# Kernel tuning notes

Measured on AMD Instinct MI355X. Metric: run time of the kernel, lower is better.

## Reference

```python
import jax, jax.numpy as jnp
import numpy as np

B, L, D = 2, 2048, 2048
H = 16
DH = D // H  # 128
EPS = 1e-6


def _rope_cos_sin(seq_len, dim, dtype):
    inv_freq = 1.0 / (10000.0 ** (jnp.arange(0, dim, 2, dtype=jnp.float32) / dim))
    t = jnp.arange(seq_len, dtype=jnp.float32)
    freqs = jnp.einsum('i,j->ij', t, inv_freq)          # [L, dim/2]
    emb = jnp.concatenate([freqs, freqs], axis=-1)      # [L, dim]
    return jnp.cos(emb).astype(dtype)[None, None], jnp.sin(emb).astype(dtype)[None, None]


def _rotate_half(x):
    x1, x2 = jnp.split(x, 2, axis=-1)
    return jnp.concatenate([-x2, x1], axis=-1)


def _rms_norm(x, w):
    var = jnp.mean(jnp.square(x), axis=-1, keepdims=True)
    return x * jax.lax.rsqrt(var + EPS) * w


def setup_inputs() -> dict:
    key = jax.random.key(0)
    ks = jax.random.split(key, 4)
    s_in = 1.0 / np.sqrt(D)
    return {
        'x': jax.random.normal(ks[0], (B, L, D), jnp.float32),
        'attention_mask': jnp.zeros((B, 1, 1, L), jnp.bool_),
        'Wqkv': jax.random.normal(ks[1], (D, 3 * D), jnp.float32) * s_in,
        'bqkv': jnp.zeros((3 * D,), jnp.float32),
        'Wout': jax.random.normal(ks[2], (D, D), jnp.float32) * s_in,
        'bout': jnp.zeros((D,), jnp.float32),
        'q_norm_w': jnp.ones((DH,), jnp.float32),
        'k_norm_w': jnp.ones((DH,), jnp.float32),
    }


def reference(x, attention_mask, Wqkv, bqkv, Wout, bout, q_norm_w, k_norm_w):
    b, l, d = x.shape
    qkv = x @ Wqkv + bqkv                                   # [B,L,3D]
    q, k, v = jnp.split(qkv, 3, axis=-1)
    # [B,H,L,DH]
    q = q.reshape(b, l, H, DH).transpose(0, 2, 1, 3)
    k = k.reshape(b, l, H, DH).transpose(0, 2, 1, 3)
    v = v.reshape(b, l, H, DH).transpose(0, 2, 1, 3)

    cos, sin = _rope_cos_sin(l, DH, x.dtype)
    q = q * cos + _rotate_half(q) * sin
    k = k * cos + _rotate_half(k) * sin

    q = _rms_norm(q, q_norm_w)
    k = _rms_norm(k, k_norm_w)

    # SDPA with additive (float-cast) mask, as in the original code
    scale = 1.0 / np.sqrt(DH)
    scores = jnp.einsum('bhqd,bhkd->bhqk', q, k) * scale
    scores = scores + attention_mask.astype(x.dtype)        # broadcast [B,1,1,L]
    attn = jax.nn.softmax(scores, axis=-1)
    out = jnp.einsum('bhqk,bhkd->bhqd', attn, v)            # [B,H,L,DH]

    # zero out masked query rows: padding_mask = mask.transpose(2,3) -> [B,1,L,1]
    padding_mask = jnp.swapaxes(attention_mask, 2, 3)
    out = jnp.where(padding_mask, 0.0, out)

    out = out.transpose(0, 2, 1, 3).reshape(b, l, d)
    return out @ Wout + bout
```

## Files before the change

kernel.cpp:

```cpp
#include <hip/hip_runtime.h>
#include <hip/hip_bf16.h>

typedef __bf16 bf16;
using bf16x8 = __attribute__((ext_vector_type(8))) __bf16;
using bf16x4 = __attribute__((ext_vector_type(4))) __bf16;
using f32x4  = __attribute__((ext_vector_type(4))) float;
using f32x16 = __attribute__((ext_vector_type(16))) float;

#define DEV __device__ __forceinline__

DEV void load_lds16(const void* g, void* l) {
  __builtin_amdgcn_global_load_lds(
      (const __attribute__((address_space(1))) void*)g,
      (__attribute__((address_space(3))) void*)l, 16, 0, 0);
}

__global__ __launch_bounds__(256) void k_prep(
    const float* __restrict__ x, bf16* __restrict__ xb,
    const float* __restrict__ Wq, bf16* __restrict__ wqT,
    const float* __restrict__ Wo, bf16* __restrict__ woT,
    float* __restrict__ invf) {
  __shared__ float t[64][65];
  int bid = blockIdx.x;
  int tid = threadIdx.x;
  if (bid < 4096) {
    long i = ((long)bid * 256 + tid) * 8;
    float4 a = *(const float4*)(x + i);
    float4 b = *(const float4*)(x + i + 4);
    bf16x8 o;
    o[0] = (bf16)a.x; o[1] = (bf16)a.y; o[2] = (bf16)a.z; o[3] = (bf16)a.w;
    o[4] = (bf16)b.x; o[5] = (bf16)b.y; o[6] = (bf16)b.z; o[7] = (bf16)b.w;
    *(bf16x8*)(xb + i) = o;
    return;
  }
  if (bid >= 8192) {
    if (tid < 64) invf[tid] = 1.0f / (float)pow(10000.0, (double)tid / 64.0);
    return;
  }
  const float* in;
  bf16* out;
  int R, C, rb;
  if (bid < 7168) { in = Wq; out = wqT; R = 2048; C = 6144; rb = bid - 4096; }
  else            { in = Wo; out = woT; R = 2048; C = 2048; rb = bid - 7168; }
  int nbc = C >> 6;
  long r0 = (long)(rb / nbc) * 64, c0 = (long)(rb % nbc) * 64;
#pragma unroll
  for (int i = 0; i < 4; ++i) {
    int ch = tid + i * 256;
    int r = ch >> 4, c4 = (ch & 15) * 4;
    float4 v = *(const float4*)(in + (r0 + r) * C + c0 + c4);
    t[r][c4] = v.x; t[r][c4 + 1] = v.y; t[r][c4 + 2] = v.z; t[r][c4 + 3] = v.w;
  }
  __syncthreads();
#pragma unroll
  for (int i = 0; i < 2; ++i) {
    int ch = tid + i * 256;
    int c = ch >> 3, r8 = (ch & 7) * 8;
    bf16x8 o;
#pragma unroll
    for (int j = 0; j < 8; ++j) o[j] = (bf16)t[r8 + j][c];
    *(bf16x8*)(out + (c0 + c) * R + r0 + r8) = o;
  }
}

template <typename OutT>
__global__ __launch_bounds__(256) void k_gemm_bt(
    const bf16* __restrict__ A, const bf16* __restrict__ Bt,
    const float* __restrict__ bias, OutT* __restrict__ C,
    int M, int N, int K, int fuse,
    const float* __restrict__ invf,
    const float* __restrict__ qw, const float* __restrict__ kw,
    bf16* __restrict__ q_r, bf16* __restrict__ k_r, bf16* __restrict__ v_t) {
  __shared__ __align__(16) bf16 lAB[2][128 * 64];
  bf16* lA = lAB[0];
  bf16* lB = lAB[1];
  int bid = blockIdx.x;
  if ((gridDim.x & 7) == 0) {
    int q = gridDim.x >> 3;
    bid = (bid & 7) * q + (bid >> 3);
  }
  int nbn = N >> 7;
  int bm = bid / nbn, bn = bid % nbn;
  const int tid = threadIdx.x, lane = tid & 63, wid = tid >> 6;
  const int wr = wid >> 1, wc = wid & 1;
  const int fr = lane & 15, fq = lane >> 4;
  const long abase = (long)bm * 128 * K, bbase = (long)bn * 128 * K;
  f32x4 acc[4][4] = {};

  for (int k0 = 0; k0 < K; k0 += 64) {
    __syncthreads();
#pragma unroll
    for (int it = 0; it < 4; ++it) {
      int ch = it * 256 + tid;
      int r = ch >> 3, u = ch & 7;
      load_lds16(A + abase + (long)r * K + k0 + ((u ^ (r & 7)) << 3), &lA[ch * 8]);
    }
#pragma unroll
    for (int it = 0; it < 4; ++it) {
      int ch = it * 256 + tid;
      int r = ch >> 3, u = ch & 7;
      load_lds16(Bt + bbase + (long)r * K + k0 + ((u ^ (r & 7)) << 3), &lB[ch * 8]);
    }
    __syncthreads();
    bf16x8 af[4][2], bf_[4][2];
#pragma unroll
    for (int m = 0; m < 4; ++m) {
      int R = wr * 64 + m * 16 + fr;
#pragma unroll
      for (int kk = 0; kk < 2; ++kk)
        af[m][kk] = *(const bf16x8*)&lA[R * 64 + (((kk * 4 + fq) ^ (R & 7)) << 3)];
    }
#pragma unroll
    for (int n = 0; n < 4; ++n) {
      int R = wc * 64 + n * 16 + fr;
#pragma unroll
      for (int kk = 0; kk < 2; ++kk)
        bf_[n][kk] = *(const bf16x8*)&lB[R * 64 + (((kk * 4 + fq) ^ (R & 7)) << 3)];
    }
#pragma unroll
    for (int m = 0; m < 4; ++m)
#pragma unroll
      for (int n = 0; n < 4; ++n)
#pragma unroll
        for (int kk = 0; kk < 2; ++kk)
          acc[m][n] = __builtin_amdgcn_mfma_f32_16x16x32_bf16(af[m][kk], bf_[n][kk],
                                                              acc[m][n], 0, 0, 0);
  }

  if (!fuse) {
#pragma unroll
    for (int n = 0; n < 4; ++n) {
      int col = bn * 128 + wc * 64 + n * 16 + fr;
      float bv = bias[col];
#pragma unroll
      for (int m = 0; m < 4; ++m) {
        int row0 = bm * 128 + wr * 64 + m * 16 + fq * 4;
#pragma unroll
        for (int r = 0; r < 4; ++r) {
          float v = acc[m][n][r] + bv;
          C[(long)(row0 + r) * N + col] = (OutT)v;
        }
      }
    }
    return;
  }

  __syncthreads();
  bf16* tile = lAB[0];
  const int h = bn & 15;
  const int b = bm >> 4, l0 = (bm & 15) << 7;

  if (bn < 32) {
#pragma unroll
    for (int n = 0; n < 4; ++n) {
      int col = wc * 64 + n * 16 + fr;
      float bv = bias[bn * 128 + col];
#pragma unroll
      for (int m = 0; m < 4; ++m)
#pragma unroll
        for (int r = 0; r < 4; ++r) {
          int row = wr * 64 + m * 16 + fq * 4 + r;
          tile[row * 128 + (col ^ ((row & 7) << 3))] = (bf16)(acc[m][n][r] + bv);
        }
    }
    __syncthreads();
    const float* wv = (bn < 16) ? qw : kw;
    bf16* dst0 = (bn < 16) ? q_r : k_r;
    const int tcol = tid & 15, rgrp = tid >> 4, i8 = tcol * 8;
    const bool lo = i8 < 64;
    float wvv[8], invv[8];
#pragma unroll
    for (int j = 0; j < 8; ++j) wvv[j] = wv[i8 + j];
#pragma unroll
    for (int j = 0; j < 8; ++j) invv[j] = invf[(i8 + j) & 63];
#pragma unroll
    for (int it = 0; it < 8; ++it) {
      int row = it * 16 + rgrp;
      float fl = (float)(l0 + row);
      float cc[8], sn[8];
#pragma unroll
      for (int j = 0; j < 8; ++j) __sincosf(fl * invv[j], &sn[j], &cc[j]);
      bf16x8 xv = *(const bf16x8*)&tile[row * 128 + (i8 ^ ((row & 7) << 3))];
      float v[8], p[8], rr[8];
      float ss = 0.f;
#pragma unroll
      for (int j = 0; j < 8; ++j) v[j] = (float)xv[j];
#pragma unroll
      for (int j = 0; j < 8; ++j) p[j] = __shfl_xor(v[j], 8);
#pragma unroll
      for (int j = 0; j < 8; ++j) {
        rr[j] = lo ? v[j] * cc[j] - p[j] * sn[j] : v[j] * cc[j] + p[j] * sn[j];
        ss += rr[j] * rr[j];
      }
      ss += __shfl_xor(ss, 1);
      ss += __shfl_xor(ss, 2);
      ss += __shfl_xor(ss, 4);
      ss += __shfl_xor(ss, 8);
      float inv = rsqrtf(ss * (1.f / 128.f) + 1e-6f);
      bf16x8 ov;
#pragma unroll
      for (int j = 0; j < 8; ++j) ov[j] = (bf16)(rr[j] * inv * wvv[j]);
      *(bf16x8*)(dst0 + ((long)((b * 16 + h) * 2048 + (l0 + row))) * 128 + i8) = ov;
    }
  } else {
#pragma unroll
    for (int n = 0; n < 4; ++n) {
      int col = wc * 64 + n * 16 + fr;
      float bv = bias[bn * 128 + col];
#pragma unroll
      for (int m = 0; m < 4; ++m)
#pragma unroll
        for (int r = 0; r < 4; ++r) {
          int row = wr * 64 + m * 16 + fq * 4 + r;
          tile[col * 128 + (row ^ ((col & 7) << 3))] = (bf16)(acc[m][n][r] + bv);
        }
    }
    __syncthreads();
    bf16* dstb = v_t + ((long)((b * 16 + h) * 128)) * 2048 + l0;
#pragma unroll
    for (int it = 0; it < 8; ++it) {
      int ch = it * 256 + tid;
      int d = ch >> 4, l8 = (ch & 15) * 8;
      bf16x8 vv = *(const bf16x8*)&tile[d * 128 + (l8 ^ ((d & 7) << 3))];
      *(bf16x8*)(dstb + (long)d * 2048 + l8) = vv;
    }
  }
}

__global__ __launch_bounds__(512, 1) void k_attn(
    const bf16* __restrict__ q_r, const bf16* __restrict__ k_r,
    const bf16* __restrict__ v_t, const unsigned char* __restrict__ amask,
    bf16* __restrict__ attno) {
  __shared__ __align__(16) bf16 lK[2][64 * 128];
  __shared__ __align__(16) bf16 lV[3][128 * 64];
  __shared__ int sAny;
  const int tid = threadIdx.x, lane = tid & 63, w = tid >> 6;
  const int hi = lane >> 5, q31 = lane & 31;
  const int bh = blockIdx.x & 31, qt = blockIdx.x >> 5;
  const int b = bh >> 4, h = bh & 15;
  const long hbase = (long)bh * 2048 * 128;
  const int q0 = qt * 256 + w * 32;
  const unsigned char* mb = amask + b * 2048;

  if (tid == 0) sAny = 0;
  __syncthreads();
  {
    unsigned mv = *(const unsigned*)(mb + tid * 4);
    if (mv) sAny = 1;
  }

  bf16x8 qf[8];
#pragma unroll
  for (int ksl = 0; ksl < 8; ++ksl)
    qf[ksl] = *(const bf16x8*)(q_r + hbase + (long)(q0 + q31) * 128 + ksl * 16 + hi * 8);

  f32x16 o[4] = {};
  float m_run = -1e30f, l_run = 0.f;
  const float SC2 = 0.08838834764831845f * 1.4426950408889634f;
  const float L2E = 1.4426950408889634f;

#define STAGE_K(buf, kv0)                                                            \
  {                                                                                  \
    _Pragma("unroll") for (int it = 0; it < 2; ++it) {                               \
      int g = it * 512 + w * 64 + lane;                                              \
      int r = g >> 4, u = g & 15;                                                    \
      load_lds16(k_r + hbase + (long)((kv0) + r) * 128 + ((u ^ (r & 7)) << 3),       \
                 &lK[buf][(it * 512 + w * 64) * 8]);                                 \
    }                                                                                \
  }
#define STAGE_V(buf, kv0)                                                            \
  {                                                                                  \
    _Pragma("unroll") for (int it = 0; it < 2; ++it) {                               \
      int g = it * 512 + w * 64 + lane;                                              \
      int r = g >> 3, u = g & 7;                                                     \
      load_lds16(v_t + hbase + (long)r * 2048 + (kv0) + ((u ^ (r & 7)) << 3),        \
                 &lV[buf][(it * 512 + w * 64) * 8]);                                 \
    }                                                                                \
  }

  STAGE_K(0, 0) STAGE_V(0, 0) STAGE_K(1, 64) STAGE_V(1, 64)
  __syncthreads();
  const bool maskAny = sAny != 0;

  f32x16 st0 = {}, st1 = {};
#pragma unroll
  for (int ksl = 0; ksl < 8; ++ksl) {
    const int u = ksl * 2 + hi;
    bf16x8 kf0 = *(const bf16x8*)&lK[0][q31 * 128 + ((u ^ (q31 & 7)) << 3)];
    bf16x8 kf1 = *(const bf16x8*)&lK[0][(32 + q31) * 128 + ((u ^ (q31 & 7)) << 3)];
    st0 = __builtin_amdgcn_mfma_f32_32x32x16_bf16(kf0, qf[ksl], st0, 0, 0, 0);
    st1 = __builtin_amdgcn_mfma_f32_32x32x16_bf16(kf1, qf[ksl], st1, 0, 0, 0);
  }
  __syncthreads();

  for (int t = 0; t < 32; ++t) {
    const int kv0 = t << 6;
    if (t + 2 < 32) {
      STAGE_K(t & 1, kv0 + 128)
      STAGE_V((t + 2) % 3, kv0 + 128)
    }

    f32x16 sn0 = {}, sn1 = {};
    if (t < 31) {
      const bf16* kb = lK[(t + 1) & 1];
#pragma unroll
      for (int ksl = 0; ksl < 8; ++ksl) {
        const int u = ksl * 2 + hi;
        bf16x8 kf0 = *(const bf16x8*)&kb[q31 * 128 + ((u ^ (q31 & 7)) << 3)];
        bf16x8 kf1 = *(const bf16x8*)&kb[(32 + q31) * 128 + ((u ^ (q31 & 7)) << 3)];
        sn0 = __builtin_amdgcn_mfma_f32_32x32x16_bf16(kf0, qf[ksl], sn0, 0, 0, 0);
        sn1 = __builtin_amdgcn_mfma_f32_32x32x16_bf16(kf1, qf[ksl], sn1, 0, 0, 0);
      }
    }

#pragma unroll
    for (int i = 0; i < 16; ++i) { st0[i] *= SC2; st1[i] *= SC2; }
    if (maskAny) {
#pragma unroll
      for (int i = 0; i < 16; ++i) {
        int c = (i & 3) + 8 * (i >> 2) + 4 * hi;
        if (mb[kv0 + c]) st0[i] += L2E;
        if (mb[kv0 + 32 + c]) st1[i] += L2E;
      }
    }
    float tm = st0[0];
#pragma unroll
    for (int i = 1; i < 16; ++i) tm = fmaxf(tm, st0[i]);
#pragma unroll
    for (int i = 0; i < 16; ++i) tm = fmaxf(tm, st1[i]);
    tm = fmaxf(tm, __shfl_xor(tm, 32));

    if (!__all(tm <= m_run + 8.f)) {
      float mn = fmaxf(m_run, tm);
      float corr = exp2f(m_run - mn);
      m_run = mn;
      l_run *= corr;
#pragma unroll
      for (int i = 0; i < 16; ++i) {
        float cr = __shfl(corr, (i & 3) + 8 * (i >> 2) + 4 * hi);
#pragma unroll
        for (int dt = 0; dt < 4; ++dt) o[dt][i] *= cr;
      }
    }

    float rs = 0.f;
#pragma unroll
    for (int i = 0; i < 16; ++i) { st0[i] = exp2f(st0[i] - m_run); rs += st0[i]; }
#pragma unroll
    for (int i = 0; i < 16; ++i) { st1[i] = exp2f(st1[i] - m_run); rs += st1[i]; }
    rs += __shfl_xor(rs, 32);
    l_run += rs;

    union UU { bf16x4 v; uint2 u; };
    union U8 { bf16x8 v; uint4 u; };
    bf16x8 pa[4];
#define MKPA(pidx, STX, bb)                                                          \
  {                                                                                  \
    UU plo, phi;                                                                     \
    plo.v = (bf16x4){(bf16)STX[bb], (bf16)STX[(bb) + 1], (bf16)STX[(bb) + 2],        \
                     (bf16)STX[(bb) + 3]};                                           \
    phi.v = (bf16x4){(bf16)STX[(bb) + 4], (bf16)STX[(bb) + 5], (bf16)STX[(bb) + 6],  \
                     (bf16)STX[(bb) + 7]};                                           \
    unsigned sx = hi ? plo.u.x : phi.u.x, sy = hi ? plo.u.y : phi.u.y;               \
    unsigned rx = (unsigned)__shfl_xor((int)sx, 32), ry = (unsigned)__shfl_xor((int)sy, 32); \
    U8 f;                                                                            \
    f.u.x = hi ? rx : plo.u.x; f.u.y = hi ? ry : plo.u.y;                            \
    f.u.z = hi ? phi.u.x : rx; f.u.w = hi ? phi.u.y : ry;                            \
    pa[pidx] = f.v;                                                                  \
  }
    MKPA(0, st0, 0) MKPA(1, st0, 8) MKPA(2, st1, 0) MKPA(3, st1, 8)
#undef MKPA

    const bf16* vb3 = lV[t % 3];
#pragma unroll
    for (int dt = 0; dt < 4; ++dt) {
      const int dr = dt * 32 + q31;
#pragma unroll
      for (int ks = 0; ks < 4; ++ks) {
        const int u = ks * 2 + hi;
        bf16x8 vb = *(const bf16x8*)&vb3[dr * 64 + ((u ^ (dr & 7)) << 3)];
        o[dt] = __builtin_amdgcn_mfma_f32_32x32x16_bf16(pa[ks], vb, o[dt], 0, 0, 0);
      }
    }

    __syncthreads();
    st0 = sn0;
    st1 = sn1;
  }
#undef STAGE_K
#undef STAGE_V

  float invl = 1.f / l_run;
#pragma unroll
  for (int i = 0; i < 16; ++i) {
    int q = (i & 3) + 8 * (i >> 2) + 4 * hi;
    int qrow = q0 + q;
    float inv = __shfl(invl, q);
    float zm = inv;
    if (maskAny) { if (mb[qrow]) zm = 0.f; }
#pragma unroll
    for (int dt = 0; dt < 4; ++dt)
      attno[(long)(b * 2048 + qrow) * 2048 + h * 128 + dt * 32 + q31] = (bf16)(o[dt][i] * zm);
  }
}

extern "C" void kernel_launch(void* const* d_in, const int* in_sizes, int n_in,
                              void* d_out, int out_size, void* d_ws, size_t ws_size,
                              hipStream_t stream) {
  const float* x = (const float*)d_in[0];
  const unsigned char* amask = (const unsigned char*)d_in[1];
  const float* Wqkv = (const float*)d_in[2];
  const float* bqkv = (const float*)d_in[3];
  const float* Wout = (const float*)d_in[4];
  const float* bout = (const float*)d_in[5];
  const float* qw = (const float*)d_in[6];
  const float* kw = (const float*)d_in[7];
  float* out = (float*)d_out;
  char* ws = (char*)d_ws;

  bf16* xb   = (bf16*)(ws);
  bf16* wqT  = (bf16*)(ws + 16777216);
  bf16* woT  = (bf16*)(ws + 41943040);
  bf16* q_r  = (bf16*)(ws + 100663296);
  bf16* k_r  = (bf16*)(ws + 117440512);
  bf16* v_t  = (bf16*)(ws + 134217728);
  float* invf = (float*)(ws + 150994944);
  bf16* attno = xb;

  k_prep<<<8193, 256, 0, stream>>>(x, xb, Wqkv, wqT, Wout, woT, invf);
  k_gemm_bt<bf16><<<32 * 48, 256, 0, stream>>>(xb, wqT, bqkv, (bf16*)nullptr,
                                               4096, 6144, 2048, 1,
                                               invf, qw, kw, q_r, k_r, v_t);
  k_attn<<<256, 512, 0, stream>>>(q_r, k_r, v_t, amask, attno);
  k_gemm_bt<float><<<32 * 16, 256, 0, stream>>>(attno, woT, bout, out,
                                                4096, 2048, 2048, 0,
                                                nullptr, nullptr, nullptr,
                                                nullptr, nullptr, nullptr);
}
```

Before: 304.2 us.

## Replace QKV GEMM with 256x256-tile, 8-wave, software-pipelined kernel

The fused QKV projection GEMM moves from 128x128 tiles with 4 waves and a load-sync-compute loop to 256x256 tiles with 8 waves. Global-to-LDS loads are double-buffered and interleaved across four compute phases, with explicit vmcnt waits, barriers and setprio around the MFMA bursts. The larger tile cuts global/LDS traffic per flop and hides load latency behind compute. The cost is 128KB of LDS, one block per CU and a grid of only 384 blocks, which may leave the 256 CUs unevenly loaded. The RoPE/RMSNorm and V-transpose epilogues are adapted to cover two heads per tile, and the output GEMM is split into its own non-templated kernel.

```diff
diff --git a/kernel.cpp b/kernel.cpp
--- a/kernel.cpp
+++ b/kernel.cpp
@@ -63,110 +63,107 @@
   }
 }
 
-template <typename OutT>
-__global__ __launch_bounds__(256) void k_gemm_bt(
+__global__ __launch_bounds__(512, 1) void k_gemm8q(
     const bf16* __restrict__ A, const bf16* __restrict__ Bt,
-    const float* __restrict__ bias, OutT* __restrict__ C,
-    int M, int N, int K, int fuse,
+    const float* __restrict__ bias,
     const float* __restrict__ invf,
     const float* __restrict__ qw, const float* __restrict__ kw,
     bf16* __restrict__ q_r, bf16* __restrict__ k_r, bf16* __restrict__ v_t) {
-  __shared__ __align__(16) bf16 lAB[2][128 * 64];
-  bf16* lA = lAB[0];
-  bf16* lB = lAB[1];
+  __shared__ __align__(16) bf16 ls[2][2][256 * 64];
   int bid = blockIdx.x;
-  if ((gridDim.x & 7) == 0) {
-    int q = gridDim.x >> 3;
-    bid = (bid & 7) * q + (bid >> 3);
-  }
-  int nbn = N >> 7;
-  int bm = bid / nbn, bn = bid % nbn;
-  const int tid = threadIdx.x, lane = tid & 63, wid = tid >> 6;
-  const int wr = wid >> 1, wc = wid & 1;
+  { int q = gridDim.x >> 3; bid = (bid & 7) * q + (bid >> 3); }
+  const int bm = bid & 15, bn = bid >> 4;
+  const int tid = threadIdx.x, lane = tid & 63, w = tid >> 6;
+  const int wm = w >> 2, wn = w & 3;
   const int fr = lane & 15, fq = lane >> 4;
-  const long abase = (long)bm * 128 * K, bbase = (long)bn * 128 * K;
-  f32x4 acc[4][4] = {};
-
-  for (int k0 = 0; k0 < K; k0 += 64) {
+  const long abase = (long)bm * 256 * 2048;
+  const long bbase = (long)bn * 256 * 2048;
+  f32x4 acc[8][4] = {};
+  bf16x8 bfv[4][2];
+
+#define STG(op, GP, gb, kt, hf)                                                \
+  { _Pragma("unroll") for (int it2 = 0; it2 < 2; ++it2) {                      \
+      int g = it2 * 512 + tid;                                                 \
+      int rl = g >> 3, u = g & 7;                                              \
+      load_lds16(GP + gb + (long)((hf) * 128 + rl) * 2048 + ((kt) << 6)        \
+                     + ((u ^ (rl & 7)) << 3),                                  \
+                 &ls[op][(kt) & 1][(hf) * 8192 + g * 8]);                      \
+  } }
+
+#define PH(qd, slot, STGCODE)                                                  \
+  {                                                                            \
+    bf16x8 afv[2][2];                                                          \
+    _Pragma("unroll") for (int mm = 0; mm < 2; ++mm)                           \
+      _Pragma("unroll") for (int kk = 0; kk < 2; ++kk) {                       \
+        int R = wm * 128 + ((qd) * 2 + mm) * 16 + fr;                          \
+        afv[mm][kk] = *(const bf16x8*)&ls[0][slot]                             \
+            [R * 64 + (((kk * 4 + fq) ^ (R & 7)) << 3)];                       \
+      }                                                                        \
+    if ((qd) == 0) {                                                           \
+      _Pragma("unroll") for (int nn = 0; nn < 4; ++nn)                         \
+        _Pragma("unroll") for (int kk = 0; kk < 2; ++kk) {                     \
+          int R = wn * 64 + nn * 16 + fr;                                      \
+          bfv[nn][kk] = *(const bf16x8*)&ls[1][slot]                           \
+              [R * 64 + (((kk * 4 + fq) ^ (R & 7)) << 3)];                     \
+        }                                                                      \
+    }                                                                          \
+    STGCODE                                                                    \
+    __builtin_amdgcn_s_barrier();                                              \
+    asm volatile("s_waitcnt lgkmcnt(0)" ::: "memory");                         \
+    __builtin_amdgcn_s_setprio(1);                                             \
+    _Pragma("unroll") for (int mm = 0; mm < 2; ++mm)                           \
+      _Pragma("unroll") for (int nn = 0; nn < 4; ++nn)                         \
+        _Pragma("unroll") for (int kk = 0; kk < 2; ++kk)                       \
+          acc[(qd) * 2 + mm][nn] = __builtin_amdgcn_mfma_f32_16x16x32_bf16(    \
+              afv[mm][kk], bfv[nn][kk], acc[(qd) * 2 + mm][nn], 0, 0, 0);      \
+    __builtin_amdgcn_s_setprio(0);                                             \
+    __builtin_amdgcn_s_barrier();                                              \
+  }
+
+  STG(1, Bt, bbase, 0, 0) STG(1, Bt, bbase, 0, 1)
+  STG(0, A, abase, 0, 0)  STG(0, A, abase, 0, 1)
+  STG(1, Bt, bbase, 1, 0) STG(1, Bt, bbase, 1, 1)
+
+  for (int u = 0; u < 16; ++u) {
+    const int t = 2 * u;
+    asm volatile("s_waitcnt vmcnt(4)" ::: "memory");
+    __builtin_amdgcn_s_barrier();
+    PH(0, 0, STG(0, A, abase, t + 1, 0))
+    PH(1, 0, STG(0, A, abase, t + 1, 1))
+    PH(2, 0, if (u < 15) { STG(1, Bt, bbase, t + 2, 0) })
+    PH(3, 0, if (u < 15) { STG(1, Bt, bbase, t + 2, 1) })
+    if (u < 15) { asm volatile("s_waitcnt vmcnt(4)" ::: "memory"); }
+    else        { asm volatile("s_waitcnt vmcnt(0)" ::: "memory"); }
+    __builtin_amdgcn_s_barrier();
+    PH(0, 1, if (u < 15) { STG(0, A, abase, t + 2, 0) })
+    PH(1, 1, if (u < 15) { STG(0, A, abase, t + 2, 1) })
+    PH(2, 1, if (u < 15) { STG(1, Bt, bbase, t + 3, 0) })
+    PH(3, 1, if (u < 15) { STG(1, Bt, bbase, t + 3, 1) })
+  }
+#undef PH
+#undef STG
+
+  bf16* tile = &ls[0][0][0];
+  const int b = bm >> 3, l0 = (bm & 7) << 8;
+
+  if (bn < 16) {
+#pragma unroll
+    for (int n = 0; n < 4; ++n) {
+      int col = wn * 64 + n * 16 + fr;
+      float bv = bias[bn * 256 + col];
+#pragma unroll
+      for (int m = 0; m < 8; ++m)
+#pragma unroll
+        for (int r = 0; r < 4; ++r) {
+          int row = wm * 128 + m * 16 + fq * 4 + r;
+          tile[row * 256 + (col ^ ((row & 7) << 3))] = (bf16)(acc[m][n][r] + bv);
+        }
+    }
     __syncthreads();
-#pragma unroll
-    for (int it = 0; it < 4; ++it) {
-      int ch = it * 256 + tid;
-      int r = ch >> 3, u = ch & 7;
-      load_lds16(A + abase + (long)r * K + k0 + ((u ^ (r & 7)) << 3), &lA[ch * 8]);
-    }
-#pragma unroll
-    for (int it = 0; it < 4; ++it) {
-      int ch = it * 256 + tid;
-      int r = ch >> 3, u = ch & 7;
-      load_lds16(Bt + bbase + (long)r * K + k0 + ((u ^ (r & 7)) << 3), &lB[ch * 8]);
-    }
-    __syncthreads();
-    bf16x8 af[4][2], bf_[4][2];
-#pragma unroll
-    for (int m = 0; m < 4; ++m) {
-      int R = wr * 64 + m * 16 + fr;
-#pragma unroll
-      for (int kk = 0; kk < 2; ++kk)
-        af[m][kk] = *(const bf16x8*)&lA[R * 64 + (((kk * 4 + fq) ^ (R & 7)) << 3)];
-    }
-#pragma unroll
-    for (int n = 0; n < 4; ++n) {
-      int R = wc * 64 + n * 16 + fr;
-#pragma unroll
-      for (int kk = 0; kk < 2; ++kk)
-        bf_[n][kk] = *(const bf16x8*)&lB[R * 64 + (((kk * 4 + fq) ^ (R & 7)) << 3)];
-    }
-#pragma unroll
-    for (int m = 0; m < 4; ++m)
-#pragma unroll
-      for (int n = 0; n < 4; ++n)
-#pragma unroll
-        for (int kk = 0; kk < 2; ++kk)
-          acc[m][n] = __builtin_amdgcn_mfma_f32_16x16x32_bf16(af[m][kk], bf_[n][kk],
-                                                              acc[m][n], 0, 0, 0);
-  }
-
-  if (!fuse) {
-#pragma unroll
-    for (int n = 0; n < 4; ++n) {
-      int col = bn * 128 + wc * 64 + n * 16 + fr;
-      float bv = bias[col];
-#pragma unroll
-      for (int m = 0; m < 4; ++m) {
-        int row0 = bm * 128 + wr * 64 + m * 16 + fq * 4;
-#pragma unroll
-        for (int r = 0; r < 4; ++r) {
-          float v = acc[m][n][r] + bv;
-          C[(long)(row0 + r) * N + col] = (OutT)v;
-        }
-      }
-    }
-    return;
-  }
-
-  __syncthreads();
-  bf16* tile = lAB[0];
-  const int h = bn & 15;
-  const int b = bm >> 4, l0 = (bm & 15) << 7;
-
-  if (bn < 32) {
-#pragma unroll
-    for (int n = 0; n < 4; ++n) {
-      int col = wc * 64 + n * 16 + fr;
-      float bv = bias[bn * 128 + col];
-#pragma unroll
-      for (int m = 0; m < 4; ++m)
-#pragma unroll
-        for (int r = 0; r < 4; ++r) {
-          int row = wr * 64 + m * 16 + fq * 4 + r;
-          tile[row * 128 + (col ^ ((row & 7) << 3))] = (bf16)(acc[m][n][r] + bv);
-        }
-    }
-    __syncthreads();
-    const float* wv = (bn < 16) ? qw : kw;
-    bf16* dst0 = (bn < 16) ? q_r : k_r;
-    const int tcol = tid & 15, rgrp = tid >> 4, i8 = tcol * 8;
+    const float* wv = (bn < 8) ? qw : kw;
+    bf16* dst0 = (bn < 8) ? q_r : k_r;
+    const int tc = tid & 15, hh = (tid >> 4) & 1, rgrp = tid >> 5, i8 = tc * 8;
+    const int hg = (bn & 7) * 2 + hh;
     const bool lo = i8 < 64;
     float wvv[8], invv[8];
 #pragma unroll
@@ -174,13 +171,14 @@
 #pragma unroll
     for (int j = 0; j < 8; ++j) invv[j] = invf[(i8 + j) & 63];
 #pragma unroll
-    for (int it = 0; it < 8; ++it) {
+    for (int it = 0; it < 16; ++it) {
       int row = it * 16 + rgrp;
       float fl = (float)(l0 + row);
       float cc[8], sn[8];
 #pragma unroll
       for (int j = 0; j < 8; ++j) __sincosf(fl * invv[j], &sn[j], &cc[j]);
-      bf16x8 xv = *(const bf16x8*)&tile[row * 128 + (i8 ^ ((row & 7) << 3))];
+      int colb = hh * 128 + i8;
+      bf16x8 xv = *(const bf16x8*)&tile[row * 256 + (colb ^ ((row & 7) << 3))];
       float v[8], p[8], rr[8];
       float ss = 0.f;
 #pragma unroll
@@ -200,29 +198,101 @@
       bf16x8 ov;
 #pragma unroll
       for (int j = 0; j < 8; ++j) ov[j] = (bf16)(rr[j] * inv * wvv[j]);
-      *(bf16x8*)(dst0 + ((long)((b * 16 + h) * 2048 + (l0 + row))) * 128 + i8) = ov;
+      *(bf16x8*)(dst0 + ((long)((b * 16 + hg) * 2048 + (l0 + row))) * 128 + i8) = ov;
     }
   } else {
 #pragma unroll
     for (int n = 0; n < 4; ++n) {
-      int col = wc * 64 + n * 16 + fr;
-      float bv = bias[bn * 128 + col];
-#pragma unroll
-      for (int m = 0; m < 4; ++m)
+      int col = wn * 64 + n * 16 + fr;
+      float bv = bias[bn * 256 + col];
+#pragma unroll
+      for (int m = 0; m < 8; ++m)
 #pragma unroll
         for (int r = 0; r < 4; ++r) {
-          int row = wr * 64 + m * 16 + fq * 4 + r;
-          tile[col * 128 + (row ^ ((col & 7) << 3))] = (bf16)(acc[m][n][r] + bv);
+          int row = wm * 128 + m * 16 + fq * 4 + r;
+          tile[col * 256 + (row ^ ((col & 7) << 3))] = (bf16)(acc[m][n][r] + bv);
         }
     }
     __syncthreads();
-    bf16* dstb = v_t + ((long)((b * 16 + h) * 128)) * 2048 + l0;
-#pragma unroll
-    for (int it = 0; it < 8; ++it) {
+#pragma unroll
+    for (int it = 0; it < 16; ++it) {
+      int ch = it * 512 + tid;
+      int d = ch >> 5, l8 = (ch & 31) * 8;
+      int hg = (bn - 16) * 2 + (d >> 7), dl = d & 127;
+      bf16x8 vv = *(const bf16x8*)&tile[d * 256 + (l8 ^ ((d & 7) << 3))];
+      *(bf16x8*)(v_t + ((long)((b * 16 + hg) * 128 + dl)) * 2048 + l0 + l8) = vv;
+    }
+  }
+}
+
+__global__ __launch_bounds__(256) void k_gemm_bt(
+    const bf16* __restrict__ A, const bf16* __restrict__ Bt,
+    const float* __restrict__ bias, float* __restrict__ C,
+    int M, int N, int K) {
+  __shared__ __align__(16) bf16 lA[128 * 64];
+  __shared__ __align__(16) bf16 lB[128 * 64];
+  int bid = blockIdx.x;
+  if ((gridDim.x & 7) == 0) {
+    int q = gridDim.x >> 3;
+    bid = (bid & 7) * q + (bid >> 3);
+  }
+  int nbn = N >> 7;
+  int bm = bid / nbn, bn = bid % nbn;
+  const int tid = threadIdx.x, lane = tid & 63, wid = tid >> 6;
+  const int wr = wid >> 1, wc = wid & 1;
+  const int fr = lane & 15, fq = lane >> 4;
+  const long abase = (long)bm * 128 * K, bbase = (long)bn * 128 * K;
+  f32x4 acc[4][4] = {};
+
+  for (int k0 = 0; k0 < K; k0 += 64) {
+    __syncthreads();
+#pragma unroll
+    for (int it = 0; it < 4; ++it) {
       int ch = it * 256 + tid;
-      int d = ch >> 4, l8 = (ch & 15) * 8;
-      bf16x8 vv = *(const bf16x8*)&tile[d * 128 + (l8 ^ ((d & 7) << 3))];
-      *(bf16x8*)(dstb + (long)d * 2048 + l8) = vv;
+      int r = ch >> 3, u = ch & 7;
+      load_lds16(A + abase + (long)r * K + k0 + ((u ^ (r & 7)) << 3), &lA[ch * 8]);
+    }
+#pragma unroll
+    for (int it = 0; it < 4; ++it) {
+      int ch = it * 256 + tid;
+      int r = ch >> 3, u = ch & 7;
+      load_lds16(Bt + bbase + (long)r * K + k0 + ((u ^ (r & 7)) << 3), &lB[ch * 8]);
+    }
+    __syncthreads();
+    bf16x8 af[4][2], bf_[4][2];
+#pragma unroll
+    for (int m = 0; m < 4; ++m) {
+      int R = wr * 64 + m * 16 + fr;
+#pragma unroll
+      for (int kk = 0; kk < 2; ++kk)
+        af[m][kk] = *(const bf16x8*)&lA[R * 64 + (((kk * 4 + fq) ^ (R & 7)) << 3)];
+    }
+#pragma unroll
+    for (int n = 0; n < 4; ++n) {
+      int R = wc * 64 + n * 16 + fr;
+#pragma unroll
+      for (int kk = 0; kk < 2; ++kk)
+        bf_[n][kk] = *(const bf16x8*)&lB[R * 64 + (((kk * 4 + fq) ^ (R & 7)) << 3)];
+    }
+#pragma unroll
+    for (int m = 0; m < 4; ++m)
+#pragma unroll
+      for (int n = 0; n < 4; ++n)
+#pragma unroll
+        for (int kk = 0; kk < 2; ++kk)
+          acc[m][n] = __builtin_amdgcn_mfma_f32_16x16x32_bf16(af[m][kk], bf_[n][kk],
+                                                              acc[m][n], 0, 0, 0);
+  }
+#pragma unroll
+  for (int n = 0; n < 4; ++n) {
+    int col = bn * 128 + wc * 64 + n * 16 + fr;
+    float bv = bias[col];
+#pragma unroll
+    for (int m = 0; m < 4; ++m) {
+      int row0 = bm * 128 + wr * 64 + m * 16 + fq * 4;
+#pragma unroll
+      for (int r = 0; r < 4; ++r)
+        C[(long)(row0 + r) * N + col] = acc[m][n][r] + bv;
     }
   }
 }
@@ -428,12 +498,7 @@
   bf16* attno = xb;
 
   k_prep<<<8193, 256, 0, stream>>>(x, xb, Wqkv, wqT, Wout, woT, invf);
-  k_gemm_bt<bf16><<<32 * 48, 256, 0, stream>>>(xb, wqT, bqkv, (bf16*)nullptr,
-                                               4096, 6144, 2048, 1,
-                                               invf, qw, kw, q_r, k_r, v_t);
+  k_gemm8q<<<384, 512, 0, stream>>>(xb, wqT, bqkv, invf, qw, kw, q_r, k_r, v_t);
   k_attn<<<256, 512, 0, stream>>>(q_r, k_r, v_t, amask, attno);
-  k_gemm_bt<float><<<32 * 16, 256, 0, stream>>>(attno, woT, bout, out,
-                                                4096, 2048, 2048, 0,
-                                                nullptr, nullptr, nullptr,
-                                                nullptr, nullptr, nullptr);
+  k_gemm_bt<<<32 * 16, 256, 0, stream>>>(attno, woT, bout, out, 4096, 2048, 2048);
 }
```

Result: faster. 289.3 us (-4.9%).

## Rewrite GEMM as 8-wave 128x256 tile with triple-buffered async LDS pipeline

Applied to the files above, without the earlier changes.

Replaces the 4-wave 128x128 GEMM with an 8-wave kernel computing 128x256 tiles. Global-to-LDS loads for the tile two steps ahead are issued while the current tile is being computed, using three LDS stages, explicit vmcnt waits and raised MFMA priority. The block mapping becomes M-major with an XCD-aware remap. The fused QKV epilogue is adapted so each block now covers two heads. This aims to hide memory latency and reuse more of each A tile, at the cost of higher LDS use, one block per CU and half as many blocks.

```diff
diff --git a/kernel.cpp b/kernel.cpp
--- a/kernel.cpp
+++ b/kernel.cpp
@@ -64,109 +64,146 @@
 }
 
 template <typename OutT>
-__global__ __launch_bounds__(256) void k_gemm_bt(
+__global__ __launch_bounds__(512, 1) void k_g8(
     const bf16* __restrict__ A, const bf16* __restrict__ Bt,
     const float* __restrict__ bias, OutT* __restrict__ C,
     int M, int N, int K, int fuse,
     const float* __restrict__ invf,
     const float* __restrict__ qw, const float* __restrict__ kw,
     bf16* __restrict__ q_r, bf16* __restrict__ k_r, bf16* __restrict__ v_t) {
-  __shared__ __align__(16) bf16 lAB[2][128 * 64];
-  bf16* lA = lAB[0];
-  bf16* lB = lAB[1];
+  __shared__ __align__(16) bf16 ls[3 * 8192 + 3 * 16384];
+  bf16* lsA = ls;
+  bf16* lsB = ls + 3 * 8192;
   int bid = blockIdx.x;
-  if ((gridDim.x & 7) == 0) {
-    int q = gridDim.x >> 3;
-    bid = (bid & 7) * q + (bid >> 3);
-  }
-  int nbn = N >> 7;
-  int bm = bid / nbn, bn = bid % nbn;
-  const int tid = threadIdx.x, lane = tid & 63, wid = tid >> 6;
-  const int wr = wid >> 1, wc = wid & 1;
+  { int q = gridDim.x >> 3; bid = (bid & 7) * q + (bid >> 3); }
+  const int nbm = M >> 7;
+  const int bm = bid % nbm, bn = bid / nbm;
+  const int tid = threadIdx.x, lane = tid & 63, w = tid >> 6;
+  const int wm = w >> 2, wn = w & 3;
   const int fr = lane & 15, fq = lane >> 4;
-  const long abase = (long)bm * 128 * K, bbase = (long)bn * 128 * K;
+  const long abase = (long)bm * 128 * K;
+  const long bbase = (long)bn * 256 * K;
+  const int NT = K >> 6;
   f32x4 acc[4][4] = {};
-
-  for (int k0 = 0; k0 < K; k0 += 64) {
+  bf16x8 bfv[4][2];
+
+#define STGA(sl, kt)                                                           \
+  { _Pragma("unroll") for (int i2 = 0; i2 < 2; ++i2) {                         \
+      int g = i2 * 512 + tid;                                                  \
+      int rl = g >> 3, uu = g & 7;                                             \
+      load_lds16(A + abase + (long)rl * K + ((kt) << 6) + ((uu ^ (rl & 7)) << 3), \
+                 &lsA[(sl) * 8192 + g * 8]); } }
+#define STGB(sl, kt, i0, i1)                                                   \
+  { _Pragma("unroll") for (int i2 = i0; i2 < i1; ++i2) {                       \
+      int g = i2 * 512 + tid;                                                  \
+      int rl = g >> 3, uu = g & 7;                                             \
+      load_lds16(Bt + bbase + (long)rl * K + ((kt) << 6) + ((uu ^ (rl & 7)) << 3), \
+                 &lsB[(sl) * 16384 + g * 8]); } }
+
+  STGA(0, 0) STGB(0, 0, 0, 4)
+  STGA(1, 1) STGB(1, 1, 0, 4)
+
+  for (int t = 0; t < NT; ++t) {
+    const int sl = t % 3, s2 = (t + 2) % 3;
+    if (t < NT - 1) asm volatile("s_waitcnt vmcnt(6)" ::: "memory");
+    else            asm volatile("s_waitcnt vmcnt(0)" ::: "memory");
+    __builtin_amdgcn_s_barrier();
+    {
+      bf16x8 af0[2][2];
+#pragma unroll
+      for (int mm = 0; mm < 2; ++mm)
+#pragma unroll
+        for (int kk = 0; kk < 2; ++kk) {
+          int R = wm * 64 + mm * 16 + fr;
+          af0[mm][kk] = *(const bf16x8*)&lsA[sl * 8192 + R * 64 + (((kk * 4 + fq) ^ (R & 7)) << 3)];
+        }
+#pragma unroll
+      for (int nn = 0; nn < 4; ++nn)
+#pragma unroll
+        for (int kk = 0; kk < 2; ++kk) {
+          int R = wn * 64 + nn * 16 + fr;
+          bfv[nn][kk] = *(const bf16x8*)&lsB[sl * 16384 + R * 64 + (((kk * 4 + fq) ^ (R & 7)) << 3)];
+        }
+      if (t + 2 < NT) { STGA(s2, t + 2) STGB(s2, t + 2, 0, 2) }
+      __builtin_amdgcn_s_barrier();
+      asm volatile("s_waitcnt lgkmcnt(0)" ::: "memory");
+      __builtin_amdgcn_s_setprio(1);
+#pragma unroll
+      for (int mm = 0; mm < 2; ++mm)
+#pragma unroll
+        for (int nn = 0; nn < 4; ++nn)
+#pragma unroll
+          for (int kk = 0; kk < 2; ++kk)
+            acc[mm][nn] = __builtin_amdgcn_mfma_f32_16x16x32_bf16(af0[mm][kk], bfv[nn][kk],
+                                                                  acc[mm][nn], 0, 0, 0);
+      __builtin_amdgcn_s_setprio(0);
+      __builtin_amdgcn_s_barrier();
+    }
+    {
+      bf16x8 af1[2][2];
+#pragma unroll
+      for (int mm = 0; mm < 2; ++mm)
+#pragma unroll
+        for (int kk = 0; kk < 2; ++kk) {
+          int R = wm * 64 + (2 + mm) * 16 + fr;
+          af1[mm][kk] = *(const bf16x8*)&lsA[sl * 8192 + R * 64 + (((kk * 4 + fq) ^ (R & 7)) << 3)];
+        }
+      if (t + 2 < NT) { STGB(s2, t + 2, 2, 4) }
+      __builtin_amdgcn_s_barrier();
+      asm volatile("s_waitcnt lgkmcnt(0)" ::: "memory");
+      __builtin_amdgcn_s_setprio(1);
+#pragma unroll
+      for (int mm = 0; mm < 2; ++mm)
+#pragma unroll
+        for (int nn = 0; nn < 4; ++nn)
+#pragma unroll
+          for (int kk = 0; kk < 2; ++kk)
+            acc[2 + mm][nn] = __builtin_amdgcn_mfma_f32_16x16x32_bf16(af1[mm][kk], bfv[nn][kk],
+                                                                      acc[2 + mm][nn], 0, 0, 0);
+      __builtin_amdgcn_s_setprio(0);
+      __builtin_amdgcn_s_barrier();
+    }
+  }
+#undef STGA
+#undef STGB
+
+  if (!fuse) {
+#pragma unroll
+    for (int nn = 0; nn < 4; ++nn) {
+      int col = bn * 256 + wn * 64 + nn * 16 + fr;
+      float bv = bias[col];
+#pragma unroll
+      for (int m = 0; m < 4; ++m) {
+        int row0 = bm * 128 + wm * 64 + m * 16 + fq * 4;
+#pragma unroll
+        for (int r = 0; r < 4; ++r)
+          C[(long)(row0 + r) * N + col] = (OutT)(acc[m][nn][r] + bv);
+      }
+    }
+    return;
+  }
+
+  bf16* tile = ls;
+  const int b = bm >> 4, l0 = (bm & 15) << 7;
+
+  if (bn < 16) {
+#pragma unroll
+    for (int nn = 0; nn < 4; ++nn) {
+      int col = wn * 64 + nn * 16 + fr;
+      float bv = bias[bn * 256 + col];
+#pragma unroll
+      for (int m = 0; m < 4; ++m)
+#pragma unroll
+        for (int r = 0; r < 4; ++r) {
+          int row = wm * 64 + m * 16 + fq * 4 + r;
+          tile[row * 256 + (col ^ ((row & 7) << 3))] = (bf16)(acc[m][nn][r] + bv);
+        }
+    }
     __syncthreads();
-#pragma unroll
-    for (int it = 0; it < 4; ++it) {
-      int ch = it * 256 + tid;
-      int r = ch >> 3, u = ch & 7;
-      load_lds16(A + abase + (long)r * K + k0 + ((u ^ (r & 7)) << 3), &lA[ch * 8]);
-    }
-#pragma unroll
-    for (int it = 0; it < 4; ++it) {
-      int ch = it * 256 + tid;
-      int r = ch >> 3, u = ch & 7;
-      load_lds16(Bt + bbase + (long)r * K + k0 + ((u ^ (r & 7)) << 3), &lB[ch * 8]);
-    }
-    __syncthreads();
-    bf16x8 af[4][2], bf_[4][2];
-#pragma unroll
-    for (int m = 0; m < 4; ++m) {
-      int R = wr * 64 + m * 16 + fr;
-#pragma unroll
-      for (int kk = 0; kk < 2; ++kk)
-        af[m][kk] = *(const bf16x8*)&lA[R * 64 + (((kk * 4 + fq) ^ (R & 7)) << 3)];
-    }
-#pragma unroll
-    for (int n = 0; n < 4; ++n) {
-      int R = wc * 64 + n * 16 + fr;
-#pragma unroll
-      for (int kk = 0; kk < 2; ++kk)
-        bf_[n][kk] = *(const bf16x8*)&lB[R * 64 + (((kk * 4 + fq) ^ (R & 7)) << 3)];
-    }
-#pragma unroll
-    for (int m = 0; m < 4; ++m)
-#pragma unroll
-      for (int n = 0; n < 4; ++n)
-#pragma unroll
-        for (int kk = 0; kk < 2; ++kk)
-          acc[m][n] = __builtin_amdgcn_mfma_f32_16x16x32_bf16(af[m][kk], bf_[n][kk],
-                                                              acc[m][n], 0, 0, 0);
-  }
-
-  if (!fuse) {
-#pragma unroll
-    for (int n = 0; n < 4; ++n) {
-      int col = bn * 128 + wc * 64 + n * 16 + fr;
-      float bv = bias[col];
-#pragma unroll
-      for (int m = 0; m < 4; ++m) {
-        int row0 = bm * 128 + wr * 64 + m * 16 + fq * 4;
-#pragma unroll
-        for (int r = 0; r < 4; ++r) {
-          float v = acc[m][n][r] + bv;
-          C[(long)(row0 + r) * N + col] = (OutT)v;
-        }
-      }
-    }
-    return;
-  }
-
-  __syncthreads();
-  bf16* tile = lAB[0];
-  const int h = bn & 15;
-  const int b = bm >> 4, l0 = (bm & 15) << 7;
-
-  if (bn < 32) {
-#pragma unroll
-    for (int n = 0; n < 4; ++n) {
-      int col = wc * 64 + n * 16 + fr;
-      float bv = bias[bn * 128 + col];
-#pragma unroll
-      for (int m = 0; m < 4; ++m)
-#pragma unroll
-        for (int r = 0; r < 4; ++r) {
-          int row = wr * 64 + m * 16 + fq * 4 + r;
-          tile[row * 128 + (col ^ ((row & 7) << 3))] = (bf16)(acc[m][n][r] + bv);
-        }
-    }
-    __syncthreads();
-    const float* wv = (bn < 16) ? qw : kw;
-    bf16* dst0 = (bn < 16) ? q_r : k_r;
-    const int tcol = tid & 15, rgrp = tid >> 4, i8 = tcol * 8;
+    const float* wv = (bn < 8) ? qw : kw;
+    bf16* dst0 = (bn < 8) ? q_r : k_r;
+    const int tc = tid & 15, hh = (tid >> 4) & 1, rgrp = tid >> 5, i8 = tc * 8;
+    const int hg = (bn & 7) * 2 + hh;
     const bool lo = i8 < 64;
     float wvv[8], invv[8];
 #pragma unroll
@@ -180,7 +217,8 @@
       float cc[8], sn[8];
 #pragma unroll
       for (int j = 0; j < 8; ++j) __sincosf(fl * invv[j], &sn[j], &cc[j]);
-      bf16x8 xv = *(const bf16x8*)&tile[row * 128 + (i8 ^ ((row & 7) << 3))];
+      int colb = hh * 128 + i8;
+      bf16x8 xv = *(const bf16x8*)&tile[row * 256 + (colb ^ ((row & 7) << 3))];
       float v[8], p[8], rr[8];
       float ss = 0.f;
 #pragma unroll
@@ -200,29 +238,29 @@
       bf16x8 ov;
 #pragma unroll
       for (int j = 0; j < 8; ++j) ov[j] = (bf16)(rr[j] * inv * wvv[j]);
-      *(bf16x8*)(dst0 + ((long)((b * 16 + h) * 2048 + (l0 + row))) * 128 + i8) = ov;
+      *(bf16x8*)(dst0 + ((long)((b * 16 + hg) * 2048 + (l0 + row))) * 128 + i8) = ov;
     }
   } else {
 #pragma unroll
-    for (int n = 0; n < 4; ++n) {
-      int col = wc * 64 + n * 16 + fr;
-      float bv = bias[bn * 128 + col];
+    for (int nn = 0; nn < 4; ++nn) {
+      int col = wn * 64 + nn * 16 + fr;
+      float bv = bias[bn * 256 + col];
 #pragma unroll
       for (int m = 0; m < 4; ++m)
 #pragma unroll
         for (int r = 0; r < 4; ++r) {
-          int row = wr * 64 + m * 16 + fq * 4 + r;
-          tile[col * 128 + (row ^ ((col & 7) << 3))] = (bf16)(acc[m][n][r] + bv);
+          int row = wm * 64 + m * 16 + fq * 4 + r;
+          tile[col * 128 + (row ^ ((col & 7) << 3))] = (bf16)(acc[m][nn][r] + bv);
         }
     }
     __syncthreads();
-    bf16* dstb = v_t + ((long)((b * 16 + h) * 128)) * 2048 + l0;
 #pragma unroll
     for (int it = 0; it < 8; ++it) {
-      int ch = it * 256 + tid;
+      int ch = it * 512 + tid;
       int d = ch >> 4, l8 = (ch & 15) * 8;
+      int hg = (bn - 16) * 2 + (d >> 7), dl = d & 127;
       bf16x8 vv = *(const bf16x8*)&tile[d * 128 + (l8 ^ ((d & 7) << 3))];
-      *(bf16x8*)(dstb + (long)d * 2048 + l8) = vv;
+      *(bf16x8*)(v_t + ((long)((b * 16 + hg) * 128 + dl)) * 2048 + l0 + l8) = vv;
     }
   }
 }
@@ -428,12 +466,12 @@
   bf16* attno = xb;
 
   k_prep<<<8193, 256, 0, stream>>>(x, xb, Wqkv, wqT, Wout, woT, invf);
-  k_gemm_bt<bf16><<<32 * 48, 256, 0, stream>>>(xb, wqT, bqkv, (bf16*)nullptr,
-                                               4096, 6144, 2048, 1,
-                                               invf, qw, kw, q_r, k_r, v_t);
+  k_g8<bf16><<<768, 512, 0, stream>>>(xb, wqT, bqkv, (bf16*)nullptr,
+                                      4096, 6144, 2048, 1,
+                                      invf, qw, kw, q_r, k_r, v_t);
   k_attn<<<256, 512, 0, stream>>>(q_r, k_r, v_t, amask, attno);
-  k_gemm_bt<float><<<32 * 16, 256, 0, stream>>>(attno, woT, bout, out,
-                                                4096, 2048, 2048, 0,
-                                                nullptr, nullptr, nullptr,
-                                                nullptr, nullptr, nullptr);
+  k_g8<float><<<256, 512, 0, stream>>>(attno, woT, bout, out,
+                                       4096, 2048, 2048, 0,
+                                       nullptr, nullptr, nullptr,
+                                       nullptr, nullptr, nullptr);
 }
```

After: 291.2 us. -4.3%, faster.
